# Optimization experiments

Hardware: AMD Instinct MI355X
Metric: run time of the kernel (lower is better)

## Reference

```python
import jax, jax.numpy as jnp
import numpy as np
from jax import lax

V, E, H, T, S = 100000, 256, 512, 9, 4096
HH = H // 2
START, STOP = 7, 8
NEG = -10000.0


def setup_inputs() -> dict:
    key = jax.random.key(0)
    ks = jax.random.split(key, 16)
    def n(k, shape, scale=0.1):
        return jax.random.normal(k, shape, jnp.float32) * scale
    sentence = jax.random.randint(ks[0], (S,), 0, V)
    embed = n(ks[1], (V, E), 1.0)
    w_ih_f = n(ks[2], (4 * HH, E)); w_hh_f = n(ks[3], (4 * HH, HH))
    b_ih_f = n(ks[4], (4 * HH,));   b_hh_f = n(ks[5], (4 * HH,))
    w_ih_b = n(ks[6], (4 * HH, E)); w_hh_b = n(ks[7], (4 * HH, HH))
    b_ih_b = n(ks[8], (4 * HH,));   b_hh_b = n(ks[9], (4 * HH,))
    h0 = n(ks[10], (2, HH), 1.0)  # init_hidden: randn (2,1,HH), batch squeezed
    c0 = n(ks[11], (2, HH), 1.0)
    W_out = n(ks[12], (T, H)); b_out = n(ks[13], (T,))
    transitions = jax.random.normal(ks[14], (T, T), jnp.float32)
    transitions = transitions.at[START, :].set(NEG).at[:, STOP].set(NEG)
    return dict(sentence=sentence, embed=embed,
                w_ih_f=w_ih_f, w_hh_f=w_hh_f, b_ih_f=b_ih_f, b_hh_f=b_hh_f,
                w_ih_b=w_ih_b, w_hh_b=w_hh_b, b_ih_b=b_ih_b, b_hh_b=b_hh_b,
                h0=h0, c0=c0, W_out=W_out, b_out=b_out, transitions=transitions)


def _lstm_dir(x_gates, h0, c0, w_hh):
    # x_gates: [S, 4*HH] = x @ w_ih.T + b_ih + b_hh (precomputed input part)
    def step(carry, xg):
        h, c = carry
        g = xg + h @ w_hh.T
        i, f, gg, o = jnp.split(g, 4)  # torch gate order: i, f, g, o
        i = jax.nn.sigmoid(i); f = jax.nn.sigmoid(f)
        gg = jnp.tanh(gg);     o = jax.nn.sigmoid(o)
        c = f * c + i * gg
        h = o * jnp.tanh(c)
        return (h, c), h
    _, hs = lax.scan(step, (h0, c0), x_gates)
    return hs  # [S, HH]


def reference(sentence, embed, w_ih_f, w_hh_f, b_ih_f, b_hh_f,
              w_ih_b, w_hh_b, b_ih_b, b_hh_b, h0, c0, W_out, b_out, transitions):
    x = embed[sentence]  # [S, E]
    # bidirectional LSTM, batch=1
    hf = _lstm_dir(x @ w_ih_f.T + b_ih_f + b_hh_f, h0[0], c0[0], w_hh_f)
    hb = _lstm_dir((x @ w_ih_b.T + b_ih_b + b_hh_b)[::-1], h0[1], c0[1], w_hh_b)[::-1]
    lstm_out = jnp.concatenate([hf, hb], axis=-1)          # [S, H]
    frames = lstm_out @ W_out.T + b_out                     # [S, T] emission scores

    # Viterbi-style decode (faithful: alpha updated by logsumexp, backpointers by argmax)
    alpha0 = jnp.full((T,), NEG, jnp.float32).at[START].set(0.0)
    def vstep(alpha, frame):
        smat = alpha[:, None] + frame[None, :] + transitions  # [T, T]
        bp = jnp.argmax(smat, axis=0)
        return jax.nn.logsumexp(smat, axis=0), bp
    alpha, bps = lax.scan(vstep, alpha0, frames)            # bps: [S, T]

    final = alpha + transitions[:, STOP]                     # [T]
    best = jnp.argmax(final)
    score = jax.nn.logsumexp(final)

    # backtrack over bps[1:] in reverse
    def bstep(tag, bp):
        nt = bp[tag]
        return nt, nt
    _, path_rev = lax.scan(bstep, best, bps[1:][::-1])
    tag_seq = jnp.concatenate([path_rev[::-1], best[None]])  # [S]
    return score, tag_seq
```

## Files before the change

kernel.cpp:

```cpp
#include <hip/hip_runtime.h>
#include <hip/hip_bf16.h>

#define SEQ   4096
#define EMB   256
#define HHID  256
#define G4    1024
#define NT    9
#define TSTART 7
#define TSTOP  8
#define NEGV  (-10000.0f)
#define POISON 0xAAAAAAAAu

#define WS_XG_F   0u
#define WS_XG_B   16777216u
#define WS_HF     33554432u
#define WS_HB     37748736u
#define WS_FRAMES 41943040u

#define PIDX(c) ((((c) >> 5) * 36) + ((c) & 31))

__global__ __launch_bounds__(256) void xgate_kernel(
    const int* __restrict__ sentence, const float* __restrict__ embed,
    const float* __restrict__ w_ih_f, const float* __restrict__ b_ih_f,
    const float* __restrict__ b_hh_f,
    const float* __restrict__ w_ih_b, const float* __restrict__ b_ih_b,
    const float* __restrict__ b_hh_b,
    float* __restrict__ xg_f, float* __restrict__ xg_b)
{
    const int st  = blockIdx.x;
    const int dir = blockIdx.y;
    const float* w  = dir ? w_ih_b : w_ih_f;
    const float* bi = dir ? b_ih_b : b_ih_f;
    const float* bh = dir ? b_hh_b : b_hh_f;
    float* xg = dir ? xg_b : xg_f;
    const int t = threadIdx.x;

    __shared__ float x_t[EMB][16];
    for (int sl = 0; sl < 16; ++sl) {
        int s   = st * 16 + sl;
        int tok = sentence[s];
        x_t[t][sl] = embed[(size_t)tok * EMB + t];
    }
    __syncthreads();

    float acc[4][16];
    #pragma unroll
    for (int q = 0; q < 4; ++q)
        #pragma unroll
        for (int sl = 0; sl < 16; ++sl) acc[q][sl] = 0.f;

    const float4* wr0 = (const float4*)(w + (size_t)(t      ) * EMB);
    const float4* wr1 = (const float4*)(w + (size_t)(t + 256) * EMB);
    const float4* wr2 = (const float4*)(w + (size_t)(t + 512) * EMB);
    const float4* wr3 = (const float4*)(w + (size_t)(t + 768) * EMB);
    #pragma unroll 2
    for (int e4 = 0; e4 < EMB / 4; ++e4) {
        float4 w0 = wr0[e4], w1 = wr1[e4], w2 = wr2[e4], w3 = wr3[e4];
        #pragma unroll
        for (int k = 0; k < 4; ++k) {
            float f0 = (k == 0) ? w0.x : (k == 1) ? w0.y : (k == 2) ? w0.z : w0.w;
            float f1 = (k == 0) ? w1.x : (k == 1) ? w1.y : (k == 2) ? w1.z : w1.w;
            float f2 = (k == 0) ? w2.x : (k == 1) ? w2.y : (k == 2) ? w2.z : w2.w;
            float f3 = (k == 0) ? w3.x : (k == 1) ? w3.y : (k == 2) ? w3.z : w3.w;
            int e = e4 * 4 + k;
            #pragma unroll
            for (int sl = 0; sl < 16; ++sl) {
                float xv = x_t[e][sl];
                acc[0][sl] += f0 * xv;
                acc[1][sl] += f1 * xv;
                acc[2][sl] += f2 * xv;
                acc[3][sl] += f3 * xv;
            }
        }
    }

    float bb0 = bi[t      ] + bh[t      ];
    float bb1 = bi[t + 256] + bh[t + 256];
    float bb2 = bi[t + 512] + bh[t + 512];
    float bb3 = bi[t + 768] + bh[t + 768];
    for (int sl = 0; sl < 16; ++sl) {
        float4 val = make_float4(acc[0][sl] + bb0, acc[1][sl] + bb1,
                                 acc[2][sl] + bb2, acc[3][sl] + bb3);
        ((float4*)(xg + (size_t)(st * 16 + sl) * G4))[t] = val;
    }
}

__global__ __launch_bounds__(256, 1) void lstm_kernel(
    const float* __restrict__ xg_f, const float* __restrict__ xg_b,
    const float* __restrict__ w_hh_f, const float* __restrict__ w_hh_b,
    const float* __restrict__ h0, const float* __restrict__ c0,
    float* __restrict__ hf, float* __restrict__ hb)
{
    const int bx    = blockIdx.x;
    const int dir   = bx >> 3;
    const int slice = bx & 7;
    const int t     = threadIdx.x;
    const int cb    = t & 7;
    const int rb    = t >> 3;
    const int unit  = slice * 32 + rb;

    const float* xg   = dir ? xg_b  : xg_f;
    const float* w_hh = dir ? w_hh_b : w_hh_f;
    float* hout = dir ? hb : hf;

    __shared__ float buf[2][288];

    float wa[128];
    #pragma unroll
    for (int q = 0; q < 4; ++q) {
        #pragma unroll
        for (int j = 0; j < 32; ++j) {
            float tmp = w_hh[(size_t)(q * HHID + unit) * HHID + cb * 32 + j];
            asm volatile("v_accvgpr_write_b32 %0, %1"
                         : "=a"(wa[q * 32 + j]) : "v"(tmp));
        }
    }

    float c_reg = 0.f;
    if (cb == 0) c_reg = c0[dir * HHID + unit];

    const bool own = (t >= slice * 32) && (t < slice * 32 + 32);

    for (int n = 0; n < SEQ; ++n) {
        const int s = dir ? (SEQ - 1 - n) : n;

        float4 xgv = make_float4(0.f, 0.f, 0.f, 0.f);
        if (cb == 0) {
            xgv = *(const float4*)(xg + (size_t)s * G4 + 4u * unit);
        }

        if (n == 0) {
            buf[0][PIDX(t)] = h0[dir * HHID + t];
        } else if (!own) {
            const int sp = dir ? (s + 1) : (s - 1);
            const unsigned int* src =
                (const unsigned int*)(hout + (size_t)sp * HHID) + t;
            unsigned v = __hip_atomic_load(src, __ATOMIC_RELAXED,
                                           __HIP_MEMORY_SCOPE_AGENT);
            if (v == POISON) {
                unsigned q0, q1, q2, q3;
                q0 = __hip_atomic_load(src, __ATOMIC_RELAXED,
                                       __HIP_MEMORY_SCOPE_AGENT);
                __builtin_amdgcn_s_sleep(2);
                q1 = __hip_atomic_load(src, __ATOMIC_RELAXED,
                                       __HIP_MEMORY_SCOPE_AGENT);
                __builtin_amdgcn_s_sleep(2);
                q2 = __hip_atomic_load(src, __ATOMIC_RELAXED,
                                       __HIP_MEMORY_SCOPE_AGENT);
                __builtin_amdgcn_s_sleep(2);
                q3 = __hip_atomic_load(src, __ATOMIC_RELAXED,
                                       __HIP_MEMORY_SCOPE_AGENT);
                for (;;) {
                    if (q0 != POISON) { v = q0; break; }
                    q0 = __hip_atomic_load(src, __ATOMIC_RELAXED,
                                           __HIP_MEMORY_SCOPE_AGENT);
                    if (q1 != POISON) { v = q1; break; }
                    q1 = __hip_atomic_load(src, __ATOMIC_RELAXED,
                                           __HIP_MEMORY_SCOPE_AGENT);
                    if (q2 != POISON) { v = q2; break; }
                    q2 = __hip_atomic_load(src, __ATOMIC_RELAXED,
                                           __HIP_MEMORY_SCOPE_AGENT);
                    if (q3 != POISON) { v = q3; break; }
                    q3 = __hip_atomic_load(src, __ATOMIC_RELAXED,
                                           __HIP_MEMORY_SCOPE_AGENT);
                }
            }
            buf[n & 1][PIDX(t)] = __uint_as_float(v);
        }
        __syncthreads();

        float a0 = 0.f, a1 = 0.f, a2 = 0.f, a3 = 0.f;
        const float4* h4 = (const float4*)(&buf[n & 1][cb * 36]);
        #pragma unroll
        for (int j4 = 0; j4 < 8; ++j4) {
            float4 hv = h4[j4];
            #pragma unroll
            for (int k = 0; k < 4; ++k) {
                float hk = (k == 0) ? hv.x : (k == 1) ? hv.y
                         : (k == 2) ? hv.z : hv.w;
                float w0, w1, w2, w3;
                asm volatile("v_accvgpr_read_b32 %0, %1"
                             : "=v"(w0) : "a"(wa[0 * 32 + j4 * 4 + k]));
                asm volatile("v_accvgpr_read_b32 %0, %1"
                             : "=v"(w1) : "a"(wa[1 * 32 + j4 * 4 + k]));
                asm volatile("v_accvgpr_read_b32 %0, %1"
                             : "=v"(w2) : "a"(wa[2 * 32 + j4 * 4 + k]));
                asm volatile("v_accvgpr_read_b32 %0, %1"
                             : "=v"(w3) : "a"(wa[3 * 32 + j4 * 4 + k]));
                a0 += w0 * hk;
                a1 += w1 * hk;
                a2 += w2 * hk;
                a3 += w3 * hk;
            }
        }

        #pragma unroll
        for (int m = 1; m <= 4; m <<= 1) {
            a0 += __shfl_xor(a0, m);
            a1 += __shfl_xor(a1, m);
            a2 += __shfl_xor(a2, m);
            a3 += __shfl_xor(a3, m);
        }

        if (cb == 0) {
            float gi = a0 + xgv.x;
            float gf = a1 + xgv.y;
            float gg = a2 + xgv.z;
            float go = a3 + xgv.w;
            float iv = 1.f / (1.f + __expf(-gi));
            float fv = 1.f / (1.f + __expf(-gf));
            float gv = 1.f - 2.f / (__expf(2.f * gg) + 1.f);
            float ov = 1.f / (1.f + __expf(-go));
            float c  = fv * c_reg + iv * gv;
            c_reg = c;
            float h  = ov * (1.f - 2.f / (__expf(2.f * c) + 1.f));
            unsigned int* dst =
                (unsigned int*)(hout + (size_t)s * HHID) + unit;
            __hip_atomic_store(dst, __float_as_uint(h), __ATOMIC_RELAXED,
                               __HIP_MEMORY_SCOPE_AGENT);
            buf[(n + 1) & 1][PIDX(unit)] = h;
        }
    }
}

__global__ __launch_bounds__(256) void frames_kernel(
    const float* __restrict__ hf, const float* __restrict__ hb,
    const float* __restrict__ W_out, const float* __restrict__ b_out,
    float* __restrict__ frames)
{
    int o = blockIdx.x * 256 + threadIdx.x;
    if (o >= SEQ * NT) return;
    int s = o / NT;
    int j = o - s * NT;
    const float4* a0 = (const float4*)(hf + (size_t)s * HHID);
    const float4* a1 = (const float4*)(hb + (size_t)s * HHID);
    const float4* w0 = (const float4*)(W_out + (size_t)j * 512);
    const float4* w1 = w0 + 64;
    float acc = 0.f;
    #pragma unroll 8
    for (int i = 0; i < 64; ++i) {
        float4 a = a0[i], b = w0[i];
        acc += a.x * b.x + a.y * b.y + a.z * b.z + a.w * b.w;
        float4 c = a1[i], d = w1[i];
        acc += c.x * d.x + c.y * d.y + c.z * d.z + c.w * d.w;
    }
    frames[o] = acc + b_out[j];
}

__device__ __forceinline__ unsigned nib_ext(unsigned lo, unsigned hi,
                                            unsigned idx)
{
    unsigned a = (lo >> ((4u * idx) & 31u)) & 15u;
    return (idx < 8u) ? a : (hi & 15u);
}

__global__ __launch_bounds__(64) void crf_kernel(
    const float* __restrict__ frames, const float* __restrict__ trans,
    float* __restrict__ dout)
{
    __shared__ float fr[512 * NT];
    __shared__ unsigned char bpl[SEQ * NT];
    const int t = threadIdx.x;
    const int tc = (t < NT) ? t : 0;

    float trow[NT];
    #pragma unroll
    for (int i = 0; i < NT; ++i) trow[i] = 0.f;
    if (t < NT) {
        #pragma unroll
        for (int i = 0; i < NT; ++i) trow[i] = trans[i * NT + t];
    }
    float alpha = (t == TSTART) ? 0.f : NEGV;

    for (int chunk = 0; chunk < 8; ++chunk) {
        const float4* src4 = (const float4*)(frames + chunk * 512 * NT);
        float4* dst4 = (float4*)fr;
        for (int idx = t; idx < 512 * NT / 4; idx += 64)
            dst4[idx] = src4[idx];
        __syncthreads();

        for (int sl = 0; sl < 512; ++sl) {
            const int s = chunk * 512 + sl;
            float v[NT];
            #pragma unroll
            for (int i = 0; i < NT; ++i)
                v[i] = __shfl(alpha, i) + trow[i];
            float m01 = fmaxf(v[0], v[1]), m23 = fmaxf(v[2], v[3]);
            float m45 = fmaxf(v[4], v[5]), m67 = fmaxf(v[6], v[7]);
            float m03 = fmaxf(m01, m23),   m47 = fmaxf(m45, m67);
            float mx  = fmaxf(fmaxf(m03, m47), v[8]);
            int am = 8;
            #pragma unroll
            for (int i = 7; i >= 0; --i)
                if (v[i] == mx) am = i;
            float sum = 0.f;
            #pragma unroll
            for (int i = 0; i < NT; ++i) sum += __expf(v[i] - mx);
            float anew = fr[sl * NT + tc] + mx + __logf(sum);
            if (t < NT) {
                bpl[s * NT + t] = (unsigned char)am;
                alpha = anew;
            }
        }
        __syncthreads();
    }

    float fin = NEGV;
    if (t < NT) fin = alpha + trans[t * NT + TSTOP];
    float f[NT];
    #pragma unroll
    for (int j = 0; j < NT; ++j) f[j] = __shfl(fin, j);

    float mx2 = f[0];
    int best = 0;
    #pragma unroll
    for (int j = 1; j < NT; ++j)
        if (f[j] > mx2) { mx2 = f[j]; best = j; }
    float sum2 = 0.f;
    #pragma unroll
    for (int j = 0; j < NT; ++j) sum2 += __expf(f[j] - mx2);
    if (t == 0) dout[0] = mx2 + __logf(sum2);

    unsigned rlo[64], rhi[64];
    {
        const int base_u = t * 64 + 1;
        #pragma unroll
        for (int i = 0; i < 64; ++i) {
            unsigned lo, hi;
            if (t == 63 && i == 63) {
                lo = 0x76543210u; hi = 8u;
            } else {
                const int u = base_u + i;
                lo = 0;
                #pragma unroll
                for (int k = 0; k < 8; ++k)
                    lo |= ((unsigned)bpl[u * NT + k]) << (4 * k);
                hi = (unsigned)bpl[u * NT + 8];
            }
            rlo[i] = lo; rhi[i] = hi;
        }
    }

    unsigned gm[NT];
    #pragma unroll
    for (int k = 0; k < NT; ++k) gm[k] = (unsigned)k;
    #pragma unroll
    for (int i = 63; i >= 0; --i) {
        #pragma unroll
        for (int k = 0; k < NT; ++k)
            gm[k] = nib_ext(rlo[i], rhi[i], gm[k]);
    }
    unsigned Glo = 0, Ghi = gm[8] & 15u;
    #pragma unroll
    for (int k = 0; k < 8; ++k) Glo |= gm[k] << (4 * k);

    int cur = best;
    int E   = best;
    for (int lx = 63; lx >= 0; --lx) {
        unsigned glo = __shfl(Glo, lx);
        unsigned ghi = __shfl(Ghi, lx);
        if (t == lx) E = cur;
        cur = (int)nib_ext(glo, ghi, (unsigned)cur);
    }

    unsigned tg = (unsigned)E;
    #pragma unroll
    for (int i = 63; i >= 0; --i) {
        tg = nib_ext(rlo[i], rhi[i], tg);
        dout[1 + t * 64 + i] = (float)tg;
    }
}

extern "C" void kernel_launch(void* const* d_in, const int* in_sizes, int n_in,
                              void* d_out, int out_size, void* d_ws, size_t ws_size,
                              hipStream_t stream)
{
    const int*   sentence = (const int*)  d_in[0];
    const float* embed    = (const float*)d_in[1];
    const float* w_ih_f   = (const float*)d_in[2];
    const float* w_hh_f   = (const float*)d_in[3];
    const float* b_ih_f   = (const float*)d_in[4];
    const float* b_hh_f   = (const float*)d_in[5];
    const float* w_ih_b   = (const float*)d_in[6];
    const float* w_hh_b   = (const float*)d_in[7];
    const float* b_ih_b   = (const float*)d_in[8];
    const float* b_hh_b   = (const float*)d_in[9];
    const float* h0       = (const float*)d_in[10];
    const float* c0       = (const float*)d_in[11];
    const float* W_out    = (const float*)d_in[12];
    const float* b_out    = (const float*)d_in[13];
    const float* trans    = (const float*)d_in[14];

    float* out = (float*)d_out;
    char*  ws  = (char*)d_ws;

    float* xg_f   = (float*)(ws + WS_XG_F);
    float* xg_b   = (float*)(ws + WS_XG_B);
    float* hf     = (float*)(ws + WS_HF);
    float* hb     = (float*)(ws + WS_HB);
    float* frames = (float*)(ws + WS_FRAMES);

    hipMemsetAsync(hf, 0xAA, 2u * SEQ * HHID * sizeof(float), stream);

    xgate_kernel<<<dim3(256, 2), 256, 0, stream>>>(
        sentence, embed, w_ih_f, b_ih_f, b_hh_f, w_ih_b, b_ih_b, b_hh_b,
        xg_f, xg_b);

    lstm_kernel<<<16, 256, 0, stream>>>(
        xg_f, xg_b, w_hh_f, w_hh_b, h0, c0, hf, hb);

    frames_kernel<<<(SEQ * NT + 255) / 256, 256, 0, stream>>>(
        hf, hb, W_out, b_out, frames);

    crf_kernel<<<1, 64, 0, stream>>>(frames, trans, out);
}
```

Baseline: 9.781 ms.

## Poll recurrent hidden state with 64-bit loads from one wave; use readlane broadcasts

The LSTM recurrence now polls the previous step's hidden vector with a single wave. Each lane issues two 64-bit atomic loads and spins until both halves are non-poison, instead of every non-owning thread doing a 32-bit spin. The block's own 32 values are also read back from global memory rather than written straight to shared memory, which may add latency on the critical path. In the CRF kernel, ds_bpermute shuffles are replaced with scalar readlane broadcasts to shorten the serial alpha update.

```diff
diff --git a/kernel.cpp b/kernel.cpp
--- a/kernel.cpp
+++ b/kernel.cpp
@@ -119,8 +119,6 @@
     float c_reg = 0.f;
     if (cb == 0) c_reg = c0[dir * HHID + unit];
 
-    const bool own = (t >= slice * 32) && (t < slice * 32 + 32);
-
     for (int n = 0; n < SEQ; ++n) {
         const int s = dir ? (SEQ - 1 - n) : n;
 
@@ -131,41 +129,34 @@
 
         if (n == 0) {
             buf[0][PIDX(t)] = h0[dir * HHID + t];
-        } else if (!own) {
+        } else if (t < 64) {
             const int sp = dir ? (s + 1) : (s - 1);
-            const unsigned int* src =
-                (const unsigned int*)(hout + (size_t)sp * HHID) + t;
-            unsigned v = __hip_atomic_load(src, __ATOMIC_RELAXED,
+            const unsigned long long* row =
+                (const unsigned long long*)(hout + (size_t)sp * HHID);
+            const unsigned long long* p0 = row + t;
+            const unsigned long long* p1 = row + 64 + t;
+            unsigned long long v0 = 0, v1 = 0;
+            bool d0 = false, d1 = false;
+            do {
+                if (!d0) {
+                    v0 = __hip_atomic_load(p0, __ATOMIC_RELAXED,
                                            __HIP_MEMORY_SCOPE_AGENT);
-            if (v == POISON) {
-                unsigned q0, q1, q2, q3;
-                q0 = __hip_atomic_load(src, __ATOMIC_RELAXED,
-                                       __HIP_MEMORY_SCOPE_AGENT);
-                __builtin_amdgcn_s_sleep(2);
-                q1 = __hip_atomic_load(src, __ATOMIC_RELAXED,
-                                       __HIP_MEMORY_SCOPE_AGENT);
-                __builtin_amdgcn_s_sleep(2);
-                q2 = __hip_atomic_load(src, __ATOMIC_RELAXED,
-                                       __HIP_MEMORY_SCOPE_AGENT);
-                __builtin_amdgcn_s_sleep(2);
-                q3 = __hip_atomic_load(src, __ATOMIC_RELAXED,
-                                       __HIP_MEMORY_SCOPE_AGENT);
-                for (;;) {
-                    if (q0 != POISON) { v = q0; break; }
-                    q0 = __hip_atomic_load(src, __ATOMIC_RELAXED,
+                    d0 = ((unsigned)v0 != POISON) &&
+                         ((unsigned)(v0 >> 32) != POISON);
+                }
+                if (!d1) {
+                    v1 = __hip_atomic_load(p1, __ATOMIC_RELAXED,
                                            __HIP_MEMORY_SCOPE_AGENT);
-                    if (q1 != POISON) { v = q1; break; }
-                    q1 = __hip_atomic_load(src, __ATOMIC_RELAXED,
-                                           __HIP_MEMORY_SCOPE_AGENT);
-                    if (q2 != POISON) { v = q2; break; }
-                    q2 = __hip_atomic_load(src, __ATOMIC_RELAXED,
-                                           __HIP_MEMORY_SCOPE_AGENT);
-                    if (q3 != POISON) { v = q3; break; }
-                    q3 = __hip_atomic_load(src, __ATOMIC_RELAXED,
-                                           __HIP_MEMORY_SCOPE_AGENT);
+                    d1 = ((unsigned)v1 != POISON) &&
+                         ((unsigned)(v1 >> 32) != POISON);
                 }
-            }
-            buf[n & 1][PIDX(t)] = __uint_as_float(v);
+            } while (!(d0 && d1));
+            const int w0i = 2 * t;
+            const int w1i = 128 + 2 * t;
+            buf[n & 1][PIDX(w0i)]     = __uint_as_float((unsigned)v0);
+            buf[n & 1][PIDX(w0i) + 1] = __uint_as_float((unsigned)(v0 >> 32));
+            buf[n & 1][PIDX(w1i)]     = __uint_as_float((unsigned)v1);
+            buf[n & 1][PIDX(w1i) + 1] = __uint_as_float((unsigned)(v1 >> 32));
         }
         __syncthreads();
 
@@ -218,7 +209,6 @@
                 (unsigned int*)(hout + (size_t)s * HHID) + unit;
             __hip_atomic_store(dst, __float_as_uint(h), __ATOMIC_RELAXED,
                                __HIP_MEMORY_SCOPE_AGENT);
-            buf[(n + 1) & 1][PIDX(unit)] = h;
         }
     }
 }
@@ -254,6 +244,12 @@
     return (idx < 8u) ? a : (hi & 15u);
 }
 
+__device__ __forceinline__ float bcast_lane(float x, int lane)
+{
+    return __uint_as_float(
+        __builtin_amdgcn_readlane(__float_as_uint(x), lane));
+}
+
 __global__ __launch_bounds__(64) void crf_kernel(
     const float* __restrict__ frames, const float* __restrict__ trans,
     float* __restrict__ dout)
@@ -284,7 +280,7 @@
             float v[NT];
             #pragma unroll
             for (int i = 0; i < NT; ++i)
-                v[i] = __shfl(alpha, i) + trow[i];
+                v[i] = bcast_lane(alpha, i) + trow[i];
             float m01 = fmaxf(v[0], v[1]), m23 = fmaxf(v[2], v[3]);
             float m45 = fmaxf(v[4], v[5]), m67 = fmaxf(v[6], v[7]);
             float m03 = fmaxf(m01, m23),   m47 = fmaxf(m45, m67);
@@ -309,7 +305,7 @@
     if (t < NT) fin = alpha + trans[t * NT + TSTOP];
     float f[NT];
     #pragma unroll
-    for (int j = 0; j < NT; ++j) f[j] = __shfl(fin, j);
+    for (int j = 0; j < NT; ++j) f[j] = bcast_lane(fin, j);
 
     float mx2 = f[0];
     int best = 0;
```

Measured after the change: 10.80 ms. +10.5%, slower.
